# Optimization experiments

Measured on AMD Instinct MI355X. Metric: run time of the kernel, lower is better.

Reference implementation:

```python
import jax, jax.numpy as jnp
import numpy as np

_EPS = 0.001
_NINF = jnp.finfo(jnp.float32).min

B, LU, LE, D, H, HD = 4, 1024, 1024, 512, 8, 64


def setup_inputs() -> dict:
    ks = jax.random.split(jax.random.key(0), 16)
    w = 1.0 / np.sqrt(D)
    inp = {
        'u_enc': jax.random.normal(ks[0], (B, LU, D), jnp.float32),
        'e_enc': jax.random.normal(ks[1], (B, LE, D), jnp.float32),
        'logit_bpp': jax.random.normal(ks[2], (LU, LE), jnp.float32),
        'ue_mask': jax.random.bernoulli(ks[3], 0.9, (B, 1, LU, LE)),
        'eu_mask': jax.random.bernoulli(ks[4], 0.9, (B, 1, LE, LU)),
        'wq_k': jax.random.normal(ks[5], (D, H, HD), jnp.float32) * w,
        'wq_b': jnp.zeros((H, HD), jnp.float32),
        'wk_k': jax.random.normal(ks[6], (D, H, HD), jnp.float32) * w,
        'wk_b': jnp.zeros((H, HD), jnp.float32),
        'wv_k': jax.random.normal(ks[7], (D, H, HD), jnp.float32) * w,
        'wv_b': jnp.zeros((H, HD), jnp.float32),
        'wo_k': jax.random.normal(ks[8], (H, HD, D), jnp.float32) * (1.0 / np.sqrt(H * HD)),
        'wo_b': jnp.zeros((D,), jnp.float32),
        'bpp_w': jnp.float32(1.0),
        'bpp_b': jnp.float32(0.0),
    }
    return inp


def reference(u_enc, e_enc, logit_bpp, ue_mask, eu_mask,
              wq_k, wq_b, wk_k, wk_b, wv_k, wv_b, wo_k, wo_b,
              bpp_w, bpp_b):
    scale = jnp.reciprocal(jnp.sqrt(jnp.float32(HD)))
    # projections: [B, L, D] @ [D, H, HD] -> [B, L, H, HD]
    q_u = scale * (jnp.einsum('bld,dhk->blhk', u_enc, wq_k) + wq_b)
    q_e = scale * (jnp.einsum('bld,dhk->blhk', e_enc, wq_k) + wq_b)
    k_u = jnp.einsum('bld,dhk->blhk', u_enc, wk_k) + wk_b
    k_e = jnp.einsum('bld,dhk->blhk', e_enc, wk_k) + wk_b

    bpp = bpp_w * logit_bpp + bpp_b                 # [LU, LE]
    bpp_t = bpp.T                                   # [LE, LU]

    # scores: [B, H, Q, K]
    ue_w = jnp.einsum('bqhd,bkhd->bhqk', q_u, k_e) + bpp[None, None]
    eu_w = jnp.einsum('bqhd,bkhd->bhqk', q_e, k_u) + bpp_t[None, None]

    ue_w = jax.nn.softmax(ue_w + (~ue_mask) * _NINF + _EPS, axis=-1)
    eu_w = jax.nn.softmax(eu_w + (~eu_mask) * _NINF + _EPS, axis=-1)

    # deterministic path: no dropout; post-softmax re-mask
    ue_w = ue_mask * ue_w
    eu_w = eu_mask * eu_w

    v_u = jnp.einsum('bld,dhk->blhk', u_enc, wv_k) + wv_b
    v_e = jnp.einsum('bld,dhk->blhk', e_enc, wv_k) + wv_b

    u_ctx = jnp.einsum('bhqk,bkhd->bqhd', ue_w, v_e)
    e_ctx = jnp.einsum('bhqk,bkhd->bqhd', eu_w, v_u)

    u_update = jnp.einsum('bqhd,hde->bqe', u_ctx, wo_k) + wo_b
    e_update = jnp.einsum('bqhd,hde->bqe', e_ctx, wo_k) + wo_b
    return (u_update, e_update)
```

## Files before the change

kernel.cpp:

```cpp
#include <hip/hip_runtime.h>
#include <hip/hip_bf16.h>
#include <cstdint>

typedef unsigned short u16;
typedef __attribute__((ext_vector_type(8))) short short8;
typedef __attribute__((ext_vector_type(4))) float floatx4;

#define MFMA16(a, b, c) __builtin_amdgcn_mfma_f32_16x16x32_bf16(a, b, c, 0, 0, 0)
#define LOG2E 1.4426950408889634f

__device__ __forceinline__ float fast_exp2(float x) {
#if __has_builtin(__builtin_amdgcn_exp2f)
  return __builtin_amdgcn_exp2f(x);
#else
  return exp2f(x);
#endif
}
__device__ __forceinline__ u16 f2bf(float v) {
  union { float f; unsigned u; } x; x.f = v;
  unsigned r = x.u + 0x7FFF + ((x.u >> 16) & 1);
  return (u16)(r >> 16);
}
__device__ __forceinline__ float bf2f(u16 v) {
  union { unsigned u; float f; } x; x.u = ((unsigned)v) << 16; return x.f;
}
__device__ __forceinline__ void gload_lds16(const u16* g, u16* l) {
  __builtin_amdgcn_global_load_lds(
      (const __attribute__((address_space(1))) unsigned int*)(g),
      (__attribute__((address_space(3))) unsigned int*)(l), 16, 0, 0);
}

__global__ __launch_bounds__(256) void cvt_bf16(const float* __restrict__ u,
                                                const float* __restrict__ e,
                                                u16* __restrict__ dst) {
  int i = (blockIdx.x * 256 + threadIdx.x) * 4;
  const float* s = blockIdx.y ? e : u;
  u16* d = dst + (size_t)blockIdx.y * 2097152;
  float4 v = *(const float4*)(s + i);
  ushort4 o = make_ushort4(f2bf(v.x), f2bf(v.y), f2bf(v.z), f2bf(v.w));
  *(ushort4*)(d + i) = o;
}

__global__ __launch_bounds__(256) void wtrans(const float* __restrict__ wq,
                                              const float* __restrict__ wk,
                                              const float* __restrict__ wv,
                                              const float* __restrict__ wo,
                                              u16* __restrict__ Wt) {
  __shared__ float tl[32][33];
  const float* src = blockIdx.z == 0 ? wq : blockIdx.z == 1 ? wk : blockIdx.z == 2 ? wv : wo;
  float scale = blockIdx.z == 0 ? 0.125f * LOG2E : 1.0f;
  u16* dst = Wt + (size_t)blockIdx.z * 262144;
  int k0 = blockIdx.x * 32, n0 = blockIdx.y * 32;
  int tx = threadIdx.x & 31, ty = threadIdx.x >> 5;
#pragma unroll
  for (int i = 0; i < 32; i += 8) tl[ty + i][tx] = src[(size_t)(k0 + ty + i) * 512 + n0 + tx];
  __syncthreads();
#pragma unroll
  for (int i = 0; i < 32; i += 8)
    dst[(size_t)(n0 + ty + i) * 512 + k0 + tx] = f2bf(scale * tl[tx][ty + i]);
}

__global__ __launch_bounds__(256) void bias_cat(const float* __restrict__ q,
                                                const float* __restrict__ k,
                                                const float* __restrict__ v,
                                                const float* __restrict__ o,
                                                float* __restrict__ dst) {
  int n = blockIdx.x * 256 + threadIdx.x;
  float val = n < 512 ? 0.125f * LOG2E * q[n]
            : n < 1024 ? k[n - 512]
            : n < 1536 ? v[n - 1024] : o[n - 1536];
  dst[n] = val;
}

__global__ __launch_bounds__(256) void bpp_t(const float* __restrict__ bpp,
                                             float* __restrict__ bppT) {
  __shared__ float tl[32][33];
  int a0 = blockIdx.x * 32, b0 = blockIdx.y * 32;
  int tx = threadIdx.x & 31, ty = threadIdx.x >> 5;
#pragma unroll
  for (int i = 0; i < 32; i += 8) tl[ty + i][tx] = bpp[(size_t)(b0 + ty + i) * 1024 + a0 + tx];
  __syncthreads();
#pragma unroll
  for (int i = 0; i < 32; i += 8) bppT[(size_t)(a0 + ty + i) * 1024 + b0 + tx] = tl[tx][ty + i];
}

__global__ __launch_bounds__(256) void build_bm(const int* __restrict__ mu,
                                                const int* __restrict__ me,
                                                const float* __restrict__ bpp,
                                                const float* __restrict__ bppT,
                                                const float* __restrict__ bw_p,
                                                const float* __restrict__ bb_p,
                                                u16* __restrict__ bm) {
  int side = blockIdx.z >> 2, b = blockIdx.z & 3;
  const int* mask = side ? me : mu;
  const float* bp = side ? bppT : bpp;
  int kc = blockIdx.x;
  int q16 = blockIdx.y * 4 + (threadIdx.x >> 6);
  int lane = threadIdx.x & 63, l15 = lane & 15, quad = lane >> 4;
  float sw = (*bw_p) * LOG2E, sb = (*bb_p) * LOG2E;
  u16 vals[32];
#pragma unroll
  for (int i = 0; i < 32; ++i) {
    int kb = i >> 2, r = i & 3;
    int q = q16 * 16 + quad * 4 + r, k = kc * 128 + kb * 16 + l15;
    int m = mask[((size_t)b * 1024 + q) * 1024 + k];
    float bv = bp[(size_t)q * 1024 + k];
    vals[i] = f2bf(m ? sw * bv + sb : -1e30f);
  }
  u16* dst = bm + ((((size_t)side * 4 + b) * 64 + q16) * 8 + kc) * 2048 + (size_t)lane * 32;
#pragma unroll
  for (int j = 0; j < 4; ++j) *(short8*)(dst + j * 8) = *(const short8*)(vals + j * 8);
}

template <int MODE>
__global__ __launch_bounds__(256) void gemm_mfma(
    const u16* __restrict__ A, const u16* __restrict__ Bt,
    const float* __restrict__ bias, float* __restrict__ outf,
    u16* __restrict__ q_o, u16* __restrict__ k_o, u16* __restrict__ v_o) {
  __shared__ u16 As[128 * 32];
  __shared__ u16 Bs[128 * 32];
  const int t = threadIdx.x, lane = t & 63, wave = t >> 6;
  const int l15 = lane & 15, quad = lane >> 4;
  const int wy = wave >> 1, wx = wave & 1;
  const int m0 = blockIdx.x * 128, n0 = blockIdx.y * 128;
  const int K = 512;

  floatx4 zero4 = {0.f, 0.f, 0.f, 0.f};
  floatx4 acc[4][4];
#pragma unroll
  for (int mi = 0; mi < 4; ++mi)
#pragma unroll
    for (int ni = 0; ni < 4; ++ni) acc[mi][ni] = zero4;

  for (int k0 = 0; k0 < K; k0 += 32) {
    __syncthreads();
    {
      int s = t;
#pragma unroll
      for (int i = 0; i < 2; ++i, s += 256) {
        int row = s >> 2, seg = s & 3;
        gload_lds16(A + (size_t)(m0 + row) * K + k0 + seg * 8, &As[s * 8]);
      }
      s = t;
#pragma unroll
      for (int i = 0; i < 2; ++i, s += 256) {
        int row = s >> 2, seg = s & 3;
        gload_lds16(Bt + (size_t)(n0 + row) * K + k0 + seg * 8, &Bs[s * 8]);
      }
    }
    __syncthreads();
    short8 af[4], bf[4];
#pragma unroll
    for (int mi = 0; mi < 4; ++mi)
      af[mi] = *(const short8*)&As[(wy * 64 + mi * 16 + l15) * 32 + quad * 8];
#pragma unroll
    for (int ni = 0; ni < 4; ++ni)
      bf[ni] = *(const short8*)&Bs[(wx * 64 + ni * 16 + l15) * 32 + quad * 8];
#pragma unroll
    for (int mi = 0; mi < 4; ++mi)
#pragma unroll
      for (int ni = 0; ni < 4; ++ni) acc[mi][ni] = MFMA16(af[mi], bf[ni], acc[mi][ni]);
  }

#pragma unroll
  for (int mi = 0; mi < 4; ++mi)
#pragma unroll
    for (int ni = 0; ni < 4; ++ni) {
      int n = n0 + wx * 64 + ni * 16 + l15;
      float bv = bias[n];
#pragma unroll
      for (int r = 0; r < 4; ++r) {
        int m = m0 + wy * 64 + mi * 16 + quad * 4 + r;
        float v = acc[mi][ni][r] + bv;
        if (MODE == 1) {
          outf[(size_t)m * 512 + n] = v;
        } else {
          int sel = n >> 9, c = n & 511;
          u16 hv = f2bf(v);
          if (sel == 0) q_o[(size_t)m * 512 + c] = hv;
          else if (sel == 1) k_o[(size_t)m * 512 + c] = hv;
          else v_o[(size_t)m * 512 + c] = hv;
        }
      }
    }
}

__global__ __launch_bounds__(256) void vt_trans(const u16* __restrict__ v_all,
                                                u16* __restrict__ vt_all) {
  __shared__ u16 tl[64][72];
  int z = blockIdx.z, half = z >> 2, b = z & 3, h = blockIdx.y, l0 = blockIdx.x * 64;
  const u16* src = v_all + (size_t)half * 2097152;
  u16* dst = vt_all + (size_t)half * 2097152;
  int t = threadIdx.x;
#pragma unroll
  for (int i = 0; i < 2; ++i) {
    int s = t + i * 256, row = s >> 3, seg = s & 7;
    *(short8*)&tl[row][seg * 8] =
        *(const short8*)(src + (size_t)(b * 1024 + l0 + row) * 512 + h * 64 + seg * 8);
  }
  __syncthreads();
#pragma unroll
  for (int i = 0; i < 2; ++i) {
    int s = t + i * 256, hd = s >> 3, seg = s & 7;
    u16 tmp[8];
#pragma unroll
    for (int j = 0; j < 8; ++j) tmp[j] = tl[seg * 8 + j][hd];
    *(short8*)(dst + ((size_t)(b * 8 + h) * 64 + hd) * 1024 + l0 + seg * 8) =
        *(const short8*)tmp;
  }
}

__global__ __launch_bounds__(256) void attn_mfma(
    const u16* __restrict__ q_all, const u16* __restrict__ k_all,
    const u16* __restrict__ vt_all, const u16* __restrict__ bm_all,
    u16* __restrict__ ctx_all) {
  __shared__ u16 Ks[2][128 * 64];
  __shared__ u16 Vs[2][64 * 128];
  __shared__ u16 Ps[4][16 * 128];
  const int t = threadIdx.x, lane = t & 63, wave = t >> 6;
  const int l15 = lane & 15, quad = lane >> 4;
  const int side = blockIdx.z >> 2, b = blockIdx.z & 3, h = blockIdx.y;
  const int q0 = blockIdx.x * 128;
  const size_t HALF = 2097152;
  const u16* Q = q_all + side * HALF;
  const u16* K = k_all + (1 - side) * HALF;
  const u16* Vt = vt_all + (1 - side) * HALF;
  const u16* bm = bm_all + side * (size_t)4194304;
  u16* ctx = ctx_all + side * HALF;
  const int qbase = q0 + wave * 32;
  const int q16_0 = qbase >> 4;

  short8 qa[2][2];
#pragma unroll
  for (int s = 0; s < 2; ++s) {
    const u16* qp = Q + (size_t)(b * 1024 + qbase + s * 16 + l15) * 512 + h * 64 + quad * 8;
    qa[s][0] = *(const short8*)qp;
    qa[s][1] = *(const short8*)(qp + 32);
  }

  short8 bones;
#pragma unroll
  for (int j = 0; j < 8; ++j) bones[j] = (short)0x3F80;

  floatx4 zero4 = {0.f, 0.f, 0.f, 0.f};
  floatx4 O[2][4], O5[2];
#pragma unroll
  for (int s = 0; s < 2; ++s) {
    O5[s] = zero4;
#pragma unroll
    for (int nb = 0; nb < 4; ++nb) O[s][nb] = zero4;
  }

#define STAGE(buf, k0)                                                              \
  {                                                                                 \
    _Pragma("unroll") for (int i = 0; i < 4; ++i) {                                 \
      int s = t + i * 256, row = s >> 3, pseg = s & 7, lseg = pseg ^ (row & 7);     \
      gload_lds16(K + (size_t)(b * 1024 + (k0) + row) * 512 + h * 64 + lseg * 8,    \
                  &Ks[buf][s * 8]);                                                 \
    }                                                                               \
    _Pragma("unroll") for (int i = 0; i < 4; ++i) {                                 \
      int s = t + i * 256, row = s >> 4, pseg = s & 15, lseg = pseg ^ (row & 15);   \
      gload_lds16(Vt + ((size_t)(b * 8 + h) * 64 + row) * 1024 + (k0) + lseg * 8,   \
                  &Vs[buf][s * 8]);                                                 \
    }                                                                               \
  }

  STAGE(0, 0)

  for (int it = 0; it < 8; ++it) {
    const int cur = it & 1;
    __syncthreads();
    if (it < 7) STAGE(cur ^ 1, it * 128 + 128)

    short8 bmv[2][4];
#pragma unroll
    for (int s = 0; s < 2; ++s) {
      const u16* bp = bm + ((((size_t)b * 64 + q16_0 + s) * 8 + it) * 64 + lane) * 32;
#pragma unroll
      for (int j = 0; j < 4; ++j) bmv[s][j] = *(const short8*)(bp + j * 8);
    }

    floatx4 S[2][8];
#pragma unroll
    for (int s = 0; s < 2; ++s)
#pragma unroll
      for (int kb = 0; kb < 8; ++kb) S[s][kb] = (floatx4){-64.f, -64.f, -64.f, -64.f};
#pragma unroll
    for (int kb = 0; kb < 8; ++kb) {
      int krow = kb * 16 + l15;
      short8 b0 = *(const short8*)&Ks[cur][krow * 64 + (quad ^ (krow & 7)) * 8];
      short8 b1 = *(const short8*)&Ks[cur][krow * 64 + ((4 + quad) ^ (krow & 7)) * 8];
#pragma unroll
      for (int s = 0; s < 2; ++s) {
        S[s][kb] = MFMA16(qa[s][0], b0, S[s][kb]);
        S[s][kb] = MFMA16(qa[s][1], b1, S[s][kb]);
      }
    }

    short8 pa[2][4];
#pragma unroll
    for (int s = 0; s < 2; ++s) {
      u16* ps = &Ps[wave][0];
#pragma unroll
      for (int kb = 0; kb < 8; ++kb) {
        float pv[4];
#pragma unroll
        for (int r = 0; r < 4; ++r) {
          int i = kb * 4 + r;
          float bmf = bf2f((u16)bmv[s][i >> 3][i & 7]);
          pv[r] = fast_exp2(S[s][kb][r] + bmf);
        }
        int seg = kb * 2 + (l15 >> 3);
#pragma unroll
        for (int r = 0; r < 4; r += 2) {
          union { __hip_bfloat162 h; u16 u[2]; } cv;
          cv.h = __float22bfloat162_rn(make_float2(pv[r], pv[r + 1]));
          int row0 = quad * 4 + r, row1 = row0 + 1;
          ps[row0 * 128 + ((seg ^ row0) & 15) * 8 + (l15 & 7)] = cv.u[0];
          ps[row1 * 128 + ((seg ^ row1) & 15) * 8 + (l15 & 7)] = cv.u[1];
        }
      }
#pragma unroll
      for (int m = 0; m < 4; ++m) {
        int seg = m * 4 + quad;
        pa[s][m] = *(const short8*)&Ps[wave][l15 * 128 + ((seg ^ l15) & 15) * 8];
      }
    }

#pragma unroll
    for (int nb = 0; nb < 4; ++nb) {
      int vrow = nb * 16 + l15;
#pragma unroll
      for (int m = 0; m < 4; ++m) {
        int seg = m * 4 + quad;
        short8 vb = *(const short8*)&Vs[cur][vrow * 128 + ((seg ^ (vrow & 15)) & 15) * 8];
        O[0][nb] = MFMA16(pa[0][m], vb, O[0][nb]);
        O[1][nb] = MFMA16(pa[1][m], vb, O[1][nb]);
      }
    }
#pragma unroll
    for (int s = 0; s < 2; ++s)
#pragma unroll
      for (int m = 0; m < 4; ++m) O5[s] = MFMA16(pa[s][m], bones, O5[s]);
  }

#pragma unroll
  for (int s = 0; s < 2; ++s)
#pragma unroll
    for (int r = 0; r < 4; ++r) {
      float l = O5[s][r];
      float inv = l > 0.f ? 1.f / l : 0.f;
      int qd = qbase + s * 16 + quad * 4 + r;
      u16* cp = ctx + (size_t)(b * 1024 + qd) * 512 + h * 64;
#pragma unroll
      for (int nb = 0; nb < 4; ++nb) cp[nb * 16 + l15] = f2bf(O[s][nb][r] * inv);
    }
}

extern "C" void kernel_launch(void* const* d_in, const int* in_sizes, int n_in,
                              void* d_out, int out_size, void* d_ws, size_t ws_size,
                              hipStream_t stream) {
  const float* u_enc = (const float*)d_in[0];
  const float* e_enc = (const float*)d_in[1];
  const float* logit_bpp = (const float*)d_in[2];
  const int* ue_mask = (const int*)d_in[3];
  const int* eu_mask = (const int*)d_in[4];
  const float* wq_k = (const float*)d_in[5];
  const float* wq_b = (const float*)d_in[6];
  const float* wk_k = (const float*)d_in[7];
  const float* wk_b = (const float*)d_in[8];
  const float* wv_k = (const float*)d_in[9];
  const float* wv_b = (const float*)d_in[10];
  const float* wo_k = (const float*)d_in[11];
  const float* wo_b = (const float*)d_in[12];
  const float* bpp_w = (const float*)d_in[13];
  const float* bpp_b = (const float*)d_in[14];

  float* out = (float*)d_out;

  u16* ws16 = (u16*)d_ws;
  u16* ab    = ws16;
  u16* Wt    = ab + 4194304;
  u16* q_all = Wt + 1048576;
  u16* k_all = q_all + 4194304;
  u16* v_all = k_all + 4194304;
  u16* ctx   = v_all + 4194304;
  u16* bm    = ctx + 4194304;
  float* bppT = (float*)(bm + 8388608);
  float* bias_all = bppT + 1048576;
  u16* vt = ab;

  cvt_bf16<<<dim3(2048, 2), 256, 0, stream>>>(u_enc, e_enc, ab);
  wtrans<<<dim3(16, 16, 4), 256, 0, stream>>>(wq_k, wk_k, wv_k, wo_k, Wt);
  bias_cat<<<8, 256, 0, stream>>>(wq_b, wk_b, wv_b, wo_b, bias_all);
  bpp_t<<<dim3(32, 32), 256, 0, stream>>>(logit_bpp, bppT);
  build_bm<<<dim3(8, 16, 8), 256, 0, stream>>>(ue_mask, eu_mask, logit_bpp, bppT,
                                               bpp_w, bpp_b, bm);

  gemm_mfma<0><<<dim3(64, 12), 256, 0, stream>>>(ab, Wt, bias_all, nullptr,
                                                 q_all, k_all, v_all);
  vt_trans<<<dim3(16, 8, 8), 256, 0, stream>>>(v_all, vt);
  attn_mfma<<<dim3(8, 8, 8), 256, 0, stream>>>(q_all, k_all, vt, bm, ctx);
  gemm_mfma<1><<<dim3(64, 4), 256, 0, stream>>>(ctx, Wt + 786432, bias_all + 1536,
                                                out, nullptr, nullptr, nullptr);
}
```

Baseline: 221.0 us.

## Shrink attention tiles, fuse prep kernels, vectorize bias-mask build

The four small preprocessing kernels are merged into one launch indexed by a flat block id. build_bm now reads mask and bpp with vectorized int4/float4 loads and reorders the result through LDS into the MFMA-fragment layout. The attention kernel drops to 16 queries per wave and 64-key tiles, and uses a 1024-block flat grid with swizzled (side, b, h, x) mapping and launch_bounds(256,4), giving more resident blocks and smaller LDS and register use. The trade-off is twice as many K/V loop iterations and barriers, plus the K/V tiles are reused across fewer query rows.

```diff
diff --git a/kernel.cpp b/kernel.cpp
--- a/kernel.cpp
+++ b/kernel.cpp
@@ -30,86 +30,92 @@
       (__attribute__((address_space(3))) unsigned int*)(l), 16, 0, 0);
 }
 
-__global__ __launch_bounds__(256) void cvt_bf16(const float* __restrict__ u,
-                                                const float* __restrict__ e,
-                                                u16* __restrict__ dst) {
-  int i = (blockIdx.x * 256 + threadIdx.x) * 4;
-  const float* s = blockIdx.y ? e : u;
-  u16* d = dst + (size_t)blockIdx.y * 2097152;
-  float4 v = *(const float4*)(s + i);
-  ushort4 o = make_ushort4(f2bf(v.x), f2bf(v.y), f2bf(v.z), f2bf(v.w));
-  *(ushort4*)(d + i) = o;
-}
-
-__global__ __launch_bounds__(256) void wtrans(const float* __restrict__ wq,
-                                              const float* __restrict__ wk,
-                                              const float* __restrict__ wv,
-                                              const float* __restrict__ wo,
-                                              u16* __restrict__ Wt) {
+__global__ __launch_bounds__(256) void prep(
+    const float* __restrict__ u, const float* __restrict__ e,
+    const float* __restrict__ wq, const float* __restrict__ wk,
+    const float* __restrict__ wv, const float* __restrict__ wo,
+    const float* __restrict__ bq, const float* __restrict__ bk,
+    const float* __restrict__ bv, const float* __restrict__ bo,
+    const float* __restrict__ bpp,
+    u16* __restrict__ ab, u16* __restrict__ Wt,
+    float* __restrict__ bppT, float* __restrict__ bias_all) {
   __shared__ float tl[32][33];
-  const float* src = blockIdx.z == 0 ? wq : blockIdx.z == 1 ? wk : blockIdx.z == 2 ? wv : wo;
-  float scale = blockIdx.z == 0 ? 0.125f * LOG2E : 1.0f;
-  u16* dst = Wt + (size_t)blockIdx.z * 262144;
-  int k0 = blockIdx.x * 32, n0 = blockIdx.y * 32;
-  int tx = threadIdx.x & 31, ty = threadIdx.x >> 5;
-#pragma unroll
-  for (int i = 0; i < 32; i += 8) tl[ty + i][tx] = src[(size_t)(k0 + ty + i) * 512 + n0 + tx];
-  __syncthreads();
-#pragma unroll
-  for (int i = 0; i < 32; i += 8)
-    dst[(size_t)(n0 + ty + i) * 512 + k0 + tx] = f2bf(scale * tl[tx][ty + i]);
-}
-
-__global__ __launch_bounds__(256) void bias_cat(const float* __restrict__ q,
-                                                const float* __restrict__ k,
-                                                const float* __restrict__ v,
-                                                const float* __restrict__ o,
-                                                float* __restrict__ dst) {
-  int n = blockIdx.x * 256 + threadIdx.x;
-  float val = n < 512 ? 0.125f * LOG2E * q[n]
-            : n < 1024 ? k[n - 512]
-            : n < 1536 ? v[n - 1024] : o[n - 1536];
-  dst[n] = val;
-}
-
-__global__ __launch_bounds__(256) void bpp_t(const float* __restrict__ bpp,
-                                             float* __restrict__ bppT) {
-  __shared__ float tl[32][33];
-  int a0 = blockIdx.x * 32, b0 = blockIdx.y * 32;
-  int tx = threadIdx.x & 31, ty = threadIdx.x >> 5;
-#pragma unroll
-  for (int i = 0; i < 32; i += 8) tl[ty + i][tx] = bpp[(size_t)(b0 + ty + i) * 1024 + a0 + tx];
-  __syncthreads();
-#pragma unroll
-  for (int i = 0; i < 32; i += 8) bppT[(size_t)(a0 + ty + i) * 1024 + b0 + tx] = tl[tx][ty + i];
-}
-
-__global__ __launch_bounds__(256) void build_bm(const int* __restrict__ mu,
-                                                const int* __restrict__ me,
-                                                const float* __restrict__ bpp,
-                                                const float* __restrict__ bppT,
-                                                const float* __restrict__ bw_p,
-                                                const float* __restrict__ bb_p,
-                                                u16* __restrict__ bm) {
-  int side = blockIdx.z >> 2, b = blockIdx.z & 3;
+  const int bid = blockIdx.x, t = threadIdx.x;
+  if (bid < 4096) {
+    int half = bid >> 11;
+    int i = ((bid & 2047) * 256 + t) * 4;
+    const float* s = half ? e : u;
+    float4 v = *(const float4*)(s + i);
+    ushort4 o = make_ushort4(f2bf(v.x), f2bf(v.y), f2bf(v.z), f2bf(v.w));
+    *(ushort4*)(ab + (size_t)half * 2097152 + i) = o;
+  } else if (bid < 5120) {
+    int i = bid - 4096;
+    int z = i >> 8, rem = i & 255;
+    const float* src = z == 0 ? wq : z == 1 ? wk : z == 2 ? wv : wo;
+    float scale = z == 0 ? 0.125f * LOG2E : 1.0f;
+    u16* dst = Wt + (size_t)z * 262144;
+    int k0 = (rem & 15) * 32, n0 = (rem >> 4) * 32;
+    int tx = t & 31, ty = t >> 5;
+#pragma unroll
+    for (int j = 0; j < 32; j += 8) tl[ty + j][tx] = src[(size_t)(k0 + ty + j) * 512 + n0 + tx];
+    __syncthreads();
+#pragma unroll
+    for (int j = 0; j < 32; j += 8)
+      dst[(size_t)(n0 + ty + j) * 512 + k0 + tx] = f2bf(scale * tl[tx][ty + j]);
+  } else if (bid < 6144) {
+    int i = bid - 5120;
+    int a0 = (i & 31) * 32, b0 = (i >> 5) * 32;
+    int tx = t & 31, ty = t >> 5;
+#pragma unroll
+    for (int j = 0; j < 32; j += 8) tl[ty + j][tx] = bpp[(size_t)(b0 + ty + j) * 1024 + a0 + tx];
+    __syncthreads();
+#pragma unroll
+    for (int j = 0; j < 32; j += 8) bppT[(size_t)(a0 + ty + j) * 1024 + b0 + tx] = tl[tx][ty + j];
+  } else {
+    int n = (bid - 6144) * 256 + t;
+    float val = n < 512 ? 0.125f * LOG2E * bq[n]
+              : n < 1024 ? bk[n - 512]
+              : n < 1536 ? bv[n - 1024] : bo[n - 1536];
+    bias_all[n] = val;
+  }
+}
+
+__global__ __launch_bounds__(256) void build_bm(
+    const int* __restrict__ mu, const int* __restrict__ me,
+    const float* __restrict__ bpp, const float* __restrict__ bppT,
+    const float* __restrict__ bw_p, const float* __restrict__ bb_p,
+    u16* __restrict__ bm) {
+  __shared__ u16 lds[2048];
+  const int kcpair = blockIdx.x, q16 = blockIdx.y;
+  const int side = blockIdx.z >> 2, b = blockIdx.z & 3;
   const int* mask = side ? me : mu;
   const float* bp = side ? bppT : bpp;
-  int kc = blockIdx.x;
-  int q16 = blockIdx.y * 4 + (threadIdx.x >> 6);
-  int lane = threadIdx.x & 63, l15 = lane & 15, quad = lane >> 4;
-  float sw = (*bw_p) * LOG2E, sb = (*bb_p) * LOG2E;
-  u16 vals[32];
-#pragma unroll
-  for (int i = 0; i < 32; ++i) {
-    int kb = i >> 2, r = i & 3;
-    int q = q16 * 16 + quad * 4 + r, k = kc * 128 + kb * 16 + l15;
-    int m = mask[((size_t)b * 1024 + q) * 1024 + k];
-    float bv = bp[(size_t)q * 1024 + k];
-    vals[i] = f2bf(m ? sw * bv + sb : -1e30f);
-  }
-  u16* dst = bm + ((((size_t)side * 4 + b) * 64 + q16) * 8 + kc) * 2048 + (size_t)lane * 32;
-#pragma unroll
-  for (int j = 0; j < 4; ++j) *(short8*)(dst + j * 8) = *(const short8*)(vals + j * 8);
+  const float sw = (*bw_p) * LOG2E, sb = (*bb_p) * LOG2E;
+  const int t = threadIdx.x;
+#pragma unroll
+  for (int ii = 0; ii < 2; ++ii) {
+    int s = t + ii * 256;
+    int q = s >> 5;
+    int kq = (s & 31) * 4;
+    int qg = q16 * 16 + q, kg = kcpair * 128 + kq;
+    int4 mv = *(const int4*)(mask + ((size_t)b * 1024 + qg) * 1024 + kg);
+    float4 bv = *(const float4*)(bp + (size_t)qg * 1024 + kg);
+    int kb = (kq >> 4) & 3, kc_loc = kq >> 6;
+    int quad = q >> 2, r = q & 3;
+    u16 o[4];
+    o[0] = f2bf(mv.x ? sw * bv.x + sb : -1e30f);
+    o[1] = f2bf(mv.y ? sw * bv.y + sb : -1e30f);
+    o[2] = f2bf(mv.z ? sw * bv.z + sb : -1e30f);
+    o[3] = f2bf(mv.w ? sw * bv.w + sb : -1e30f);
+#pragma unroll
+    for (int j = 0; j < 4; ++j) {
+      int l15 = (kq & 15) + j;
+      lds[kc_loc * 1024 + (quad * 16 + l15) * 16 + kb * 4 + r] = o[j];
+    }
+  }
+  __syncthreads();
+  u16* dst = bm + ((((size_t)side * 4 + b) * 64 + q16) * 16 + kcpair * 2) * 1024;
+  *(short8*)(dst + t * 8) = *(const short8*)&lds[t * 8];
 }
 
 template <int MODE>
@@ -210,151 +216,128 @@
   }
 }
 
-__global__ __launch_bounds__(256) void attn_mfma(
+__global__ __launch_bounds__(256, 4) void attn_mfma(
     const u16* __restrict__ q_all, const u16* __restrict__ k_all,
     const u16* __restrict__ vt_all, const u16* __restrict__ bm_all,
     u16* __restrict__ ctx_all) {
-  __shared__ u16 Ks[2][128 * 64];
-  __shared__ u16 Vs[2][64 * 128];
-  __shared__ u16 Ps[4][16 * 128];
+  __shared__ u16 Ks[2][64 * 64];
+  __shared__ u16 Vs[2][64 * 64];
+  __shared__ u16 Ps[4][16 * 64];
   const int t = threadIdx.x, lane = t & 63, wave = t >> 6;
   const int l15 = lane & 15, quad = lane >> 4;
-  const int side = blockIdx.z >> 2, b = blockIdx.z & 3, h = blockIdx.y;
-  const int q0 = blockIdx.x * 128;
+
+  const int f = blockIdx.x;
+  const int g = f & 7, r0 = f >> 3;
+  const int combo = g * 8 + (r0 >> 4);
+  const int x = r0 & 15;
+  const int side = combo >> 5, b = (combo >> 3) & 3, h = combo & 7;
+
   const size_t HALF = 2097152;
   const u16* Q = q_all + side * HALF;
   const u16* K = k_all + (1 - side) * HALF;
   const u16* Vt = vt_all + (1 - side) * HALF;
   const u16* bm = bm_all + side * (size_t)4194304;
   u16* ctx = ctx_all + side * HALF;
-  const int qbase = q0 + wave * 32;
-  const int q16_0 = qbase >> 4;
-
-  short8 qa[2][2];
-#pragma unroll
-  for (int s = 0; s < 2; ++s) {
-    const u16* qp = Q + (size_t)(b * 1024 + qbase + s * 16 + l15) * 512 + h * 64 + quad * 8;
-    qa[s][0] = *(const short8*)qp;
-    qa[s][1] = *(const short8*)(qp + 32);
+  const int qbase = x * 64 + wave * 16;
+  const int q16g = qbase >> 4;
+
+  short8 qa0, qa1;
+  {
+    const u16* qp = Q + (size_t)(b * 1024 + qbase + l15) * 512 + h * 64 + quad * 8;
+    qa0 = *(const short8*)qp;
+    qa1 = *(const short8*)(qp + 32);
   }
 
   short8 bones;
 #pragma unroll
   for (int j = 0; j < 8; ++j) bones[j] = (short)0x3F80;
 
-  floatx4 zero4 = {0.f, 0.f, 0.f, 0.f};
-  floatx4 O[2][4], O5[2];
-#pragma unroll
-  for (int s = 0; s < 2; ++s) {
-    O5[s] = zero4;
-#pragma unroll
-    for (int nb = 0; nb < 4; ++nb) O[s][nb] = zero4;
-  }
-
-#define STAGE(buf, k0)                                                              \
-  {                                                                                 \
-    _Pragma("unroll") for (int i = 0; i < 4; ++i) {                                 \
-      int s = t + i * 256, row = s >> 3, pseg = s & 7, lseg = pseg ^ (row & 7);     \
-      gload_lds16(K + (size_t)(b * 1024 + (k0) + row) * 512 + h * 64 + lseg * 8,    \
-                  &Ks[buf][s * 8]);                                                 \
-    }                                                                               \
-    _Pragma("unroll") for (int i = 0; i < 4; ++i) {                                 \
-      int s = t + i * 256, row = s >> 4, pseg = s & 15, lseg = pseg ^ (row & 15);   \
-      gload_lds16(Vt + ((size_t)(b * 8 + h) * 64 + row) * 1024 + (k0) + lseg * 8,   \
-                  &Vs[buf][s * 8]);                                                 \
-    }                                                                               \
+  floatx4 O[4], O5;
+  O5 = (floatx4){0.f, 0.f, 0.f, 0.f};
+#pragma unroll
+  for (int nb = 0; nb < 4; ++nb) O[nb] = (floatx4){0.f, 0.f, 0.f, 0.f};
+
+#define STAGE(buf, k0)                                                             \
+  {                                                                                \
+    _Pragma("unroll") for (int i = 0; i < 2; ++i) {                                \
+      int s = t + i * 256, row = s >> 3, pseg = s & 7, lseg = pseg ^ (row & 7);    \
+      gload_lds16(K + (size_t)(b * 1024 + (k0) + row) * 512 + h * 64 + lseg * 8,   \
+                  &Ks[buf][s * 8]);                                                \
+      gload_lds16(Vt + ((size_t)(b * 8 + h) * 64 + row) * 1024 + (k0) + lseg * 8,  \
+                  &Vs[buf][s * 8]);                                                \
+    }                                                                              \
   }
 
   STAGE(0, 0)
 
-  for (int it = 0; it < 8; ++it) {
+  for (int it = 0; it < 16; ++it) {
     const int cur = it & 1;
     __syncthreads();
-    if (it < 7) STAGE(cur ^ 1, it * 128 + 128)
-
-    short8 bmv[2][4];
-#pragma unroll
-    for (int s = 0; s < 2; ++s) {
-      const u16* bp = bm + ((((size_t)b * 64 + q16_0 + s) * 8 + it) * 64 + lane) * 32;
-#pragma unroll
-      for (int j = 0; j < 4; ++j) bmv[s][j] = *(const short8*)(bp + j * 8);
-    }
-
-    floatx4 S[2][8];
-#pragma unroll
-    for (int s = 0; s < 2; ++s)
-#pragma unroll
-      for (int kb = 0; kb < 8; ++kb) S[s][kb] = (floatx4){-64.f, -64.f, -64.f, -64.f};
-#pragma unroll
-    for (int kb = 0; kb < 8; ++kb) {
+    if (it < 15) STAGE(cur ^ 1, it * 64 + 64)
+
+    short8 bmv0, bmv1;
+    {
+      const u16* bp = bm + ((((size_t)b * 64 + q16g) * 16 + it) * 64 + lane) * 16;
+      bmv0 = *(const short8*)bp;
+      bmv1 = *(const short8*)(bp + 8);
+    }
+
+    floatx4 S[4];
+#pragma unroll
+    for (int kb = 0; kb < 4; ++kb) S[kb] = (floatx4){-64.f, -64.f, -64.f, -64.f};
+#pragma unroll
+    for (int kb = 0; kb < 4; ++kb) {
       int krow = kb * 16 + l15;
-      short8 b0 = *(const short8*)&Ks[cur][krow * 64 + (quad ^ (krow & 7)) * 8];
-      short8 b1 = *(const short8*)&Ks[cur][krow * 64 + ((4 + quad) ^ (krow & 7)) * 8];
-#pragma unroll
-      for (int s = 0; s < 2; ++s) {
-        S[s][kb] = MFMA16(qa[s][0], b0, S[s][kb]);
-        S[s][kb] = MFMA16(qa[s][1], b1, S[s][kb]);
-      }
-    }
-
-    short8 pa[2][4];
-#pragma unroll
-    for (int s = 0; s < 2; ++s) {
-      u16* ps = &Ps[wave][0];
-#pragma unroll
-      for (int kb = 0; kb < 8; ++kb) {
-        float pv[4];
-#pragma unroll
-        for (int r = 0; r < 4; ++r) {
-          int i = kb * 4 + r;
-          float bmf = bf2f((u16)bmv[s][i >> 3][i & 7]);
-          pv[r] = fast_exp2(S[s][kb][r] + bmf);
-        }
-        int seg = kb * 2 + (l15 >> 3);
-#pragma unroll
-        for (int r = 0; r < 4; r += 2) {
-          union { __hip_bfloat162 h; u16 u[2]; } cv;
-          cv.h = __float22bfloat162_rn(make_float2(pv[r], pv[r + 1]));
-          int row0 = quad * 4 + r, row1 = row0 + 1;
-          ps[row0 * 128 + ((seg ^ row0) & 15) * 8 + (l15 & 7)] = cv.u[0];
-          ps[row1 * 128 + ((seg ^ row1) & 15) * 8 + (l15 & 7)] = cv.u[1];
-        }
-      }
-#pragma unroll
-      for (int m = 0; m < 4; ++m) {
-        int seg = m * 4 + quad;
-        pa[s][m] = *(const short8*)&Ps[wave][l15 * 128 + ((seg ^ l15) & 15) * 8];
-      }
-    }
+      short8 b0 = *(const short8*)&Ks[cur][krow * 64 + ((quad ^ (krow & 7)) * 8)];
+      short8 b1 = *(const short8*)&Ks[cur][krow * 64 + (((4 + quad) ^ (krow & 7)) * 8)];
+      S[kb] = MFMA16(qa0, b0, S[kb]);
+      S[kb] = MFMA16(qa1, b1, S[kb]);
+    }
+
+    u16* ps = &Ps[wave][0];
+#pragma unroll
+    for (int kb = 0; kb < 4; ++kb) {
+      float pv[4];
+#pragma unroll
+      for (int r = 0; r < 4; ++r) {
+        int i = kb * 4 + r;
+        float bmf = bf2f((u16)((i < 8) ? bmv0[i] : bmv1[i - 8]));
+        pv[r] = fast_exp2(S[kb][r] + bmf);
+      }
+      int seg = kb * 2 + (l15 >> 3);
+#pragma unroll
+      for (int r = 0; r < 4; r += 2) {
+        union { __hip_bfloat162 hh; u16 u[2]; } cv;
+        cv.hh = __float22bfloat162_rn(make_float2(pv[r], pv[r + 1]));
+        int row0 = quad * 4 + r, row1 = row0 + 1;
+        ps[row0 * 64 + ((seg ^ (row0 & 7)) * 8) + (l15 & 7)] = cv.u[0];
+        ps[row1 * 64 + ((seg ^ (row1 & 7)) * 8) + (l15 & 7)] = cv.u[1];
+      }
+    }
+    short8 pa0 = *(const short8*)&ps[l15 * 64 + ((quad ^ (l15 & 7)) * 8)];
+    short8 pa1 = *(const short8*)&ps[l15 * 64 + (((4 + quad) ^ (l15 & 7)) * 8)];
 
 #pragma unroll
     for (int nb = 0; nb < 4; ++nb) {
       int vrow = nb * 16 + l15;
-#pragma unroll
-      for (int m = 0; m < 4; ++m) {
-        int seg = m * 4 + quad;
-        short8 vb = *(const short8*)&Vs[cur][vrow * 128 + ((seg ^ (vrow & 15)) & 15) * 8];
-        O[0][nb] = MFMA16(pa[0][m], vb, O[0][nb]);
-        O[1][nb] = MFMA16(pa[1][m], vb, O[1][nb]);
-      }
-    }
-#pragma unroll
-    for (int s = 0; s < 2; ++s)
-#pragma unroll
-      for (int m = 0; m < 4; ++m) O5[s] = MFMA16(pa[s][m], bones, O5[s]);
-  }
-
-#pragma unroll
-  for (int s = 0; s < 2; ++s)
-#pragma unroll
-    for (int r = 0; r < 4; ++r) {
-      float l = O5[s][r];
-      float inv = l > 0.f ? 1.f / l : 0.f;
-      int qd = qbase + s * 16 + quad * 4 + r;
-      u16* cp = ctx + (size_t)(b * 1024 + qd) * 512 + h * 64;
-#pragma unroll
-      for (int nb = 0; nb < 4; ++nb) cp[nb * 16 + l15] = f2bf(O[s][nb][r] * inv);
-    }
+      short8 v0 = *(const short8*)&Vs[cur][vrow * 64 + ((quad ^ (vrow & 7)) * 8)];
+      short8 v1 = *(const short8*)&Vs[cur][vrow * 64 + (((4 + quad) ^ (vrow & 7)) * 8)];
+      O[nb] = MFMA16(pa0, v0, O[nb]);
+      O[nb] = MFMA16(pa1, v1, O[nb]);
+    }
+    O5 = MFMA16(pa0, bones, O5);
+    O5 = MFMA16(pa1, bones, O5);
+  }
+
+#pragma unroll
+  for (int r = 0; r < 4; ++r) {
+    float l = O5[r];
+    float inv = l > 0.f ? 1.f / l : 0.f;
+    int qd = qbase + quad * 4 + r;
+    u16* cp = ctx + (size_t)(b * 1024 + qd) * 512 + h * 64;
+#pragma unroll
+    for (int nb = 0; nb < 4; ++nb) cp[nb * 16 + l15] = f2bf(O[nb][r] * inv);
+  }
 }
 
 extern "C" void kernel_launch(void* const* d_in, const int* in_sizes, int n_in,
@@ -390,17 +373,15 @@
   float* bias_all = bppT + 1048576;
   u16* vt = ab;
 
-  cvt_bf16<<<dim3(2048, 2), 256, 0, stream>>>(u_enc, e_enc, ab);
-  wtrans<<<dim3(16, 16, 4), 256, 0, stream>>>(wq_k, wk_k, wv_k, wo_k, Wt);
-  bias_cat<<<8, 256, 0, stream>>>(wq_b, wk_b, wv_b, wo_b, bias_all);
-  bpp_t<<<dim3(32, 32), 256, 0, stream>>>(logit_bpp, bppT);
-  build_bm<<<dim3(8, 16, 8), 256, 0, stream>>>(ue_mask, eu_mask, logit_bpp, bppT,
+  prep<<<6152, 256, 0, stream>>>(u_enc, e_enc, wq_k, wk_k, wv_k, wo_k,
+                                 wq_b, wk_b, wv_b, wo_b, logit_bpp,
+                                 ab, Wt, bppT, bias_all);
+  build_bm<<<dim3(8, 64, 8), 256, 0, stream>>>(ue_mask, eu_mask, logit_bpp, bppT,
                                                bpp_w, bpp_b, bm);
-
   gemm_mfma<0><<<dim3(64, 12), 256, 0, stream>>>(ab, Wt, bias_all, nullptr,
                                                  q_all, k_all, v_all);
   vt_trans<<<dim3(16, 8, 8), 256, 0, stream>>>(v_all, vt);
-  attn_mfma<<<dim3(8, 8, 8), 256, 0, stream>>>(q_all, k_all, vt, bm, ctx);
+  attn_mfma<<<1024, 256, 0, stream>>>(q_all, k_all, vt, bm, ctx);
   gemm_mfma<1><<<dim3(64, 4), 256, 0, stream>>>(ctx, Wt + 786432, bias_all + 1536,
                                                 out, nullptr, nullptr, nullptr);
 }
```

Result: faster. 203.4 us (-8.0%).
